# Optimization experiments

Hardware: AMD Instinct MI355X
Metric: run time of the kernel (lower is better)

## Reference

```python
import jax, jax.numpy as jnp
import numpy as np

EPS = 1e-6
LN_EPS = 1e-6


def _bd(x, W):
    # Block-diagonal dense: x (B, F) viewed as (B, H, D); W (H, D, D)
    B = x.shape[0]
    H, D, _ = W.shape
    return jnp.einsum('bhd,hde->bhe', x.reshape(B, H, D), W).reshape(B, H * D)


def setup_inputs() -> dict:
    key = jax.random.key(0)
    B, F, H, D, K = 4096, 1024, 4, 256, 4
    ks = jax.random.split(key, 24)
    inp = {}
    inp['inputs'] = jax.random.normal(ks[0], (B, F), jnp.float32)
    inp['c'] = jax.random.normal(ks[1], (B, F), jnp.float32)
    inp['n'] = jax.random.uniform(ks[2], (B, F), jnp.float32)  # nonzero -> general stabilizer branch
    inp['m'] = jax.random.normal(ks[3], (B, F), jnp.float32)
    inp['h'] = jax.random.normal(ks[4], (B, F), jnp.float32)
    inp['conv_state'] = jax.random.normal(ks[5], (B, K, F), jnp.float32)
    inp['conv_kernel'] = jax.random.normal(ks[6], (K, F), jnp.float32) * 0.1
    inp['conv_bias'] = jax.random.normal(ks[7], (F,), jnp.float32) * 0.1
    for idx, name in enumerate(['Wi', 'Wf', 'Wz', 'Wo', 'Ri', 'Rf', 'Rz', 'Ro']):
        inp[name] = jax.random.normal(ks[8 + idx], (H, D, D), jnp.float32) * 0.02
    for idx, name in enumerate(['bi', 'bf', 'bz', 'bo']):
        inp[name] = jax.random.normal(ks[16 + idx], (F,), jnp.float32) * 0.1
    inp['ln_scale'] = jnp.ones((H, D), jnp.float32)
    return inp


def reference(inputs, c, n, m, h, conv_state, conv_kernel, conv_bias,
              Wi, Wf, Wz, Wo, Ri, Rf, Rz, Ro, bi, bf, bz, bo, ln_scale):
    B = inputs.shape[0]
    H, D = ln_scale.shape

    # Causal depthwise conv, single step: shift state, append new input
    new_conv_state = jnp.concatenate([conv_state[:, 1:, :], inputs[:, None, :]], axis=1)  # (B,K,F)
    conv_x = jnp.einsum('bkf,kf->bf', new_conv_state, conv_kernel) + conv_bias
    conv_act = jax.nn.silu(conv_x)

    # Gate pre-activations: input (block-diag) + recurrent (block-diag) + bias
    i = _bd(conv_act, Wi) + _bd(h, Ri) + bi
    f = _bd(conv_act, Wf) + _bd(h, Rf) + bf
    z = _bd(inputs, Wz) + _bd(h, Rz) + bz
    o = _bd(inputs, Wo) + _bd(h, Ro) + bo

    o_gate = jax.nn.sigmoid(o)
    log_f = -jax.nn.softplus(-f)  # forget_activation == 'sigmoid'

    # Stabilizer
    m_new = jnp.where(jnp.all(n == 0.0), i, jnp.maximum(log_f + m, i))
    i_p = jnp.minimum(jnp.exp(i - m_new), 1.0)
    f_p = jnp.minimum(jnp.exp(log_f + m - m_new), 1.0)

    c_new = f_p * c + i_p * jnp.tanh(z)
    n_new = f_p * n + i_p
    h_new = o_gate * (c_new / jnp.maximum(n_new, EPS))

    # Multi-head LayerNorm over head_dim (scale only, no bias)
    y = h_new.reshape(B, H, D)
    mu = jnp.mean(y, axis=-1, keepdims=True)
    var = jnp.var(y, axis=-1, keepdims=True)
    out = ((y - mu) * jax.lax.rsqrt(var + LN_EPS) * ln_scale).reshape(B, H * D)

    return (out, c_new, n_new, m_new, h_new, new_conv_state)
```

## Files before the change

kernel.cpp:

```cpp
#include <hip/hip_runtime.h>

#define B_N 4096
#define F_N 1024
#define H_N 4
#define D_N 256
#define BF_ELEMS (B_N * F_N)

typedef unsigned short u16;
typedef __bf16 bf16x8 __attribute__((ext_vector_type(8)));
typedef float f32x4 __attribute__((ext_vector_type(4)));
typedef u16 u16x4 __attribute__((ext_vector_type(4)));

__device__ __forceinline__ u16 f2bf(float v) {
    union { float f; unsigned u; } x; x.f = v;
    unsigned r = x.u + 0x7fffu + ((x.u >> 16) & 1u);
    return (u16)(r >> 16);
}

__global__ void kzero_flag(int* flag) {
    if (threadIdx.x == 0) *flag = 0;
}

__global__ void kflag(const float* __restrict__ n, int* __restrict__ flag) {
    int idx = blockIdx.x * 256 + threadIdx.x;
    const f32x4 v = *(const f32x4*)(n + idx * 4);
    bool any = (v[0] != 0.f) || (v[1] != 0.f) || (v[2] != 0.f) || (v[3] != 0.f);
    unsigned long long msk = __ballot(any);
    if (msk && (threadIdx.x & 63) == 0) *flag = 1;
}

__global__ void kconv(const float* __restrict__ inputs, const float* __restrict__ cs,
                      const float* __restrict__ ck, const float* __restrict__ cb,
                      const float* __restrict__ h,
                      float* __restrict__ ncs_out, u16* __restrict__ convact,
                      u16* __restrict__ hbf, u16* __restrict__ inbf) {
    int idx = blockIdx.x * 256 + threadIdx.x;
    int flat = idx << 2;
    int b = flat >> 10;
    int f = flat & 1023;
    const f32x4 x  = *(const f32x4*)(inputs + flat);
    const f32x4 c1 = *(const f32x4*)(cs + b * 4096 + 1024 + f);
    const f32x4 c2 = *(const f32x4*)(cs + b * 4096 + 2048 + f);
    const f32x4 c3 = *(const f32x4*)(cs + b * 4096 + 3072 + f);
    const f32x4 k0 = *(const f32x4*)(ck + f);
    const f32x4 k1 = *(const f32x4*)(ck + 1024 + f);
    const f32x4 k2 = *(const f32x4*)(ck + 2048 + f);
    const f32x4 k3 = *(const f32x4*)(ck + 3072 + f);
    const f32x4 bias = *(const f32x4*)(cb + f);
    const f32x4 h4 = *(const f32x4*)(h + flat);

    u16x4 ca, hb, ib;
    #pragma unroll
    for (int q = 0; q < 4; ++q) {
        float v = c1[q] * k0[q] + c2[q] * k1[q] + c3[q] * k2[q] + x[q] * k3[q] + bias[q];
        float a = v / (1.f + expf(-v));
        ca[q] = f2bf(a);
        hb[q] = f2bf(h4[q]);
        ib[q] = f2bf(x[q]);
    }
    *(u16x4*)(convact + flat) = ca;
    *(u16x4*)(hbf + flat) = hb;
    *(u16x4*)(inbf + flat) = ib;

    float* ob = ncs_out + b * 4096 + f;
    *(f32x4*)(ob)        = c1;
    *(f32x4*)(ob + 1024) = c2;
    *(f32x4*)(ob + 2048) = c3;
    *(f32x4*)(ob + 3072) = x;
}

__global__ void kconvw(const float* W0, const float* W1, const float* W2, const float* W3,
                       const float* W4, const float* W5, const float* W6, const float* W7,
                       u16* __restrict__ wt) {
    const float* tab[8] = {W0, W1, W2, W3, W4, W5, W6, W7};
    int mat = blockIdx.z;
    int hd = blockIdx.y;
    const float* src = tab[mat] + hd * 65536;
    u16* dst = wt + (mat * 4 + hd) * 65536;
    __shared__ float tile[32][33];
    int tx = threadIdx.x & 31, ty = threadIdx.x >> 5;
    int bx = (blockIdx.x & 7) * 32;
    int by = (blockIdx.x >> 3) * 32;
    #pragma unroll
    for (int r = 0; r < 4; ++r)
        tile[ty + r * 8][tx] = src[(by + ty + r * 8) * 256 + bx + tx];
    __syncthreads();
    #pragma unroll
    for (int r = 0; r < 4; ++r)
        dst[(bx + ty + r * 8) * 256 + by + tx] = f2bf(tile[tx][ty + r * 8]);
}

__global__ __launch_bounds__(256) void kgemm(
    const u16* __restrict__ convact, const u16* __restrict__ inbf,
    const u16* __restrict__ hbf, const u16* __restrict__ wt,
    float* __restrict__ gates) {
    __shared__ u16 ldsA[128 * 32];
    __shared__ u16 ldsB[64 * 32];

    int t = threadIdx.x;
    int mtile = blockIdx.x;
    int nt = blockIdx.y;
    int z = blockIdx.z;
    int pass = z >> 2;
    int hd = z & 3;
    int gsel = pass * 2 + (nt >> 2);
    int e0 = (nt & 3) * 64;
    int row0 = mtile * 128;

    const u16* a0 = (pass ? inbf : convact) + row0 * 1024 + hd * 256;
    const u16* a1 = hbf + row0 * 1024 + hd * 256;
    const u16* b0 = wt + (gsel * 4 + hd) * 65536 + e0 * 256;
    const u16* b1 = wt + ((gsel + 4) * 4 + hd) * 65536 + e0 * 256;

    f32x4 acc[4][2];
    #pragma unroll
    for (int i = 0; i < 4; ++i)
        #pragma unroll
        for (int j = 0; j < 2; ++j)
            acc[i][j] = (f32x4){0.f, 0.f, 0.f, 0.f};

    int lane = t & 63;
    int lr = lane & 15, lk = lane >> 4;
    int w = t >> 6;
    int wm = w >> 1, wn = w & 1;
    int wbase = t & ~63;

    for (int ks = 0; ks < 16; ++ks) {
        int kk = ks * 32;
        const u16* ap = (kk < 256) ? (a0 + kk) : (a1 + (kk - 256));
        const u16* bp = (kk < 256) ? (b0 + kk) : (b1 + (kk - 256));
        __syncthreads();
        #pragma unroll
        for (int s = 0; s < 2; ++s) {
            int idx = t + s * 256;
            int row = idx >> 2, seg = idx & 3;
            __builtin_amdgcn_global_load_lds(
                (const __attribute__((address_space(1))) void*)(ap + row * 1024 + seg * 8),
                (__attribute__((address_space(3))) void*)(&ldsA[(wbase + s * 256) * 8]),
                16, 0, 0);
        }
        {
            int row = t >> 2, seg = t & 3;
            __builtin_amdgcn_global_load_lds(
                (const __attribute__((address_space(1))) void*)(bp + row * 256 + seg * 8),
                (__attribute__((address_space(3))) void*)(&ldsB[wbase * 8]),
                16, 0, 0);
        }
        __syncthreads();

        bf16x8 a[4], bfr[2];
        #pragma unroll
        for (int mi = 0; mi < 4; ++mi)
            a[mi] = *(const bf16x8*)&ldsA[(wm * 64 + mi * 16 + lr) * 32 + lk * 8];
        #pragma unroll
        for (int ni = 0; ni < 2; ++ni)
            bfr[ni] = *(const bf16x8*)&ldsB[(wn * 32 + ni * 16 + lr) * 32 + lk * 8];
        #pragma unroll
        for (int mi = 0; mi < 4; ++mi)
            #pragma unroll
            for (int ni = 0; ni < 2; ++ni)
                acc[mi][ni] = __builtin_amdgcn_mfma_f32_16x16x32_bf16(a[mi], bfr[ni], acc[mi][ni], 0, 0, 0);
    }

    float* gout = gates + (size_t)gsel * BF_ELEMS;
    #pragma unroll
    for (int mi = 0; mi < 4; ++mi)
        #pragma unroll
        for (int ni = 0; ni < 2; ++ni)
            #pragma unroll
            for (int r = 0; r < 4; ++r) {
                int row = row0 + wm * 64 + mi * 16 + lk * 4 + r;
                int col = hd * 256 + e0 + wn * 32 + ni * 16 + lr;
                gout[row * 1024 + col] = acc[mi][ni][r];
            }
}

__global__ __launch_bounds__(256) void kpoint(
    const float* __restrict__ gates,
    const float* __restrict__ c, const float* __restrict__ n, const float* __restrict__ m,
    const float* __restrict__ bgi, const float* __restrict__ bgf,
    const float* __restrict__ bgz, const float* __restrict__ bgo,
    const float* __restrict__ ln_scale, const int* __restrict__ flagp,
    float* __restrict__ out) {
    int b = blockIdx.x;
    int t = threadIdx.x;
    int l = t & 63;
    int j = (t >> 6) * 256 + l * 4;
    int idx = b * 1024 + j;
    int flag = *flagp;

    f32x4 iv = *(const f32x4*)(gates + idx);
    f32x4 fv = *(const f32x4*)(gates + (size_t)BF_ELEMS + idx);
    f32x4 zv = *(const f32x4*)(gates + 2 * (size_t)BF_ELEMS + idx);
    f32x4 ov = *(const f32x4*)(gates + 3 * (size_t)BF_ELEMS + idx);
    f32x4 b_i = *(const f32x4*)(bgi + j);
    f32x4 b_f = *(const f32x4*)(bgf + j);
    f32x4 b_z = *(const f32x4*)(bgz + j);
    f32x4 b_o = *(const f32x4*)(bgo + j);
    f32x4 cv = *(const f32x4*)(c + idx);
    f32x4 nv = *(const f32x4*)(n + idx);
    f32x4 mv = *(const f32x4*)(m + idx);
    f32x4 sc = *(const f32x4*)(ln_scale + j);

    f32x4 cn, nn, mn, hn;
    float s = 0.f, ss = 0.f;
    #pragma unroll
    for (int q = 0; q < 4; ++q) {
        float I = iv[q] + b_i[q];
        float Fg = fv[q] + b_f[q];
        float Z = zv[q] + b_z[q];
        float O = ov[q] + b_o[q];
        float og = 1.f / (1.f + expf(-O));
        float lf = (Fg >= 0.f) ? -log1pf(expf(-Fg)) : (Fg - log1pf(expf(Fg)));
        float mnew = flag ? fmaxf(lf + mv[q], I) : I;
        float ip = fminf(expf(I - mnew), 1.f);
        float fp = fminf(expf(lf + mv[q] - mnew), 1.f);
        float cnew = fp * cv[q] + ip * tanhf(Z);
        float nnew = fp * nv[q] + ip;
        float hnew = og * (cnew / fmaxf(nnew, 1e-6f));
        cn[q] = cnew; nn[q] = nnew; mn[q] = mnew; hn[q] = hnew;
        s += hnew; ss += hnew * hnew;
    }
    #pragma unroll
    for (int off = 32; off >= 1; off >>= 1) {
        s  += __shfl_xor(s, off);
        ss += __shfl_xor(ss, off);
    }
    float mu = s * (1.f / 256.f);
    float var = ss * (1.f / 256.f) - mu * mu;
    float rs = rsqrtf(var + 1e-6f);

    f32x4 o4;
    #pragma unroll
    for (int q = 0; q < 4; ++q)
        o4[q] = (hn[q] - mu) * rs * sc[q];

    *(f32x4*)(out + idx) = o4;
    *(f32x4*)(out + (size_t)BF_ELEMS + idx) = cn;
    *(f32x4*)(out + 2 * (size_t)BF_ELEMS + idx) = nn;
    *(f32x4*)(out + 3 * (size_t)BF_ELEMS + idx) = mn;
    *(f32x4*)(out + 4 * (size_t)BF_ELEMS + idx) = hn;
}

extern "C" void kernel_launch(void* const* d_in, const int* in_sizes, int n_in,
                              void* d_out, int out_size, void* d_ws, size_t ws_size,
                              hipStream_t stream) {
    const float* inputs = (const float*)d_in[0];
    const float* c = (const float*)d_in[1];
    const float* n = (const float*)d_in[2];
    const float* m = (const float*)d_in[3];
    const float* h = (const float*)d_in[4];
    const float* conv_state = (const float*)d_in[5];
    const float* conv_kernel = (const float*)d_in[6];
    const float* conv_bias = (const float*)d_in[7];
    const float* W[8];
    for (int i = 0; i < 8; ++i) W[i] = (const float*)d_in[8 + i];
    const float* bgi = (const float*)d_in[16];
    const float* bgf = (const float*)d_in[17];
    const float* bgz = (const float*)d_in[18];
    const float* bgo = (const float*)d_in[19];
    const float* ln_scale = (const float*)d_in[20];
    float* out = (float*)d_out;

    char* ws = (char*)d_ws;
    int* flag = (int*)ws;
    u16* convact = (u16*)(ws + 256);
    u16* hbf = convact + BF_ELEMS;
    u16* inbf = hbf + BF_ELEMS;
    u16* wt = inbf + BF_ELEMS;
    float* gates = (float*)(ws + 256 + (size_t)3 * BF_ELEMS * 2 + (size_t)8 * 4 * 65536 * 2);

    kzero_flag<<<1, 64, 0, stream>>>(flag);
    kflag<<<4096, 256, 0, stream>>>(n, flag);
    kconv<<<4096, 256, 0, stream>>>(inputs, conv_state, conv_kernel, conv_bias, h,
                                    out + 5 * (size_t)BF_ELEMS, convact, hbf, inbf);
    kconvw<<<dim3(64, 4, 8), 256, 0, stream>>>(W[0], W[1], W[2], W[3], W[4], W[5], W[6], W[7], wt);
    kgemm<<<dim3(32, 8, 8), 256, 0, stream>>>(convact, inbf, hbf, wt, gates);
    kpoint<<<4096, 256, 0, stream>>>(gates, c, n, m, bgi, bgf, bgz, bgo, ln_scale, flag, out);
}
```

Before: 135.4 us.

## Widen GEMM N-tile, fuse bias into epilogue, store gate preactivations as bf16

New measurement: 127.0 us. 1.07x faster.

```diff
diff --git a/kernel.cpp b/kernel.cpp
--- a/kernel.cpp
+++ b/kernel.cpp
@@ -15,6 +15,11 @@
     union { float f; unsigned u; } x; x.f = v;
     unsigned r = x.u + 0x7fffu + ((x.u >> 16) & 1u);
     return (u16)(r >> 16);
+}
+
+__device__ __forceinline__ float bf2f(u16 v) {
+    union { unsigned u; float f; } x; x.u = ((unsigned)v) << 16;
+    return x.f;
 }
 
 __global__ void kzero_flag(int* flag) {
@@ -93,9 +98,11 @@
 __global__ __launch_bounds__(256) void kgemm(
     const u16* __restrict__ convact, const u16* __restrict__ inbf,
     const u16* __restrict__ hbf, const u16* __restrict__ wt,
-    float* __restrict__ gates) {
+    const float* __restrict__ bgi, const float* __restrict__ bgf,
+    const float* __restrict__ bgz, const float* __restrict__ bgo,
+    u16* __restrict__ gates16) {
     __shared__ u16 ldsA[128 * 32];
-    __shared__ u16 ldsB[64 * 32];
+    __shared__ u16 ldsB[128 * 32];
 
     int t = threadIdx.x;
     int mtile = blockIdx.x;
@@ -103,20 +110,22 @@
     int z = blockIdx.z;
     int pass = z >> 2;
     int hd = z & 3;
-    int gsel = pass * 2 + (nt >> 2);
-    int e0 = (nt & 3) * 64;
+    int gsel = pass * 2 + (nt >> 1);
+    int e0 = (nt & 1) * 128;
     int row0 = mtile * 128;
 
     const u16* a0 = (pass ? inbf : convact) + row0 * 1024 + hd * 256;
     const u16* a1 = hbf + row0 * 1024 + hd * 256;
     const u16* b0 = wt + (gsel * 4 + hd) * 65536 + e0 * 256;
     const u16* b1 = wt + ((gsel + 4) * 4 + hd) * 65536 + e0 * 256;
-
-    f32x4 acc[4][2];
+    const float* btab[4] = {bgi, bgf, bgz, bgo};
+    const float* bias = btab[gsel] + hd * 256 + e0;
+
+    f32x4 acc[4][4];
     #pragma unroll
     for (int i = 0; i < 4; ++i)
         #pragma unroll
-        for (int j = 0; j < 2; ++j)
+        for (int j = 0; j < 4; ++j)
             acc[i][j] = (f32x4){0.f, 0.f, 0.f, 0.f};
 
     int lane = t & 63;
@@ -139,47 +148,52 @@
                 (__attribute__((address_space(3))) void*)(&ldsA[(wbase + s * 256) * 8]),
                 16, 0, 0);
         }
-        {
-            int row = t >> 2, seg = t & 3;
+        #pragma unroll
+        for (int s = 0; s < 2; ++s) {
+            int idx = t + s * 256;
+            int row = idx >> 2, seg = idx & 3;
             __builtin_amdgcn_global_load_lds(
                 (const __attribute__((address_space(1))) void*)(bp + row * 256 + seg * 8),
-                (__attribute__((address_space(3))) void*)(&ldsB[wbase * 8]),
+                (__attribute__((address_space(3))) void*)(&ldsB[(wbase + s * 256) * 8]),
                 16, 0, 0);
         }
         __syncthreads();
 
-        bf16x8 a[4], bfr[2];
+        bf16x8 a[4], bfr[4];
         #pragma unroll
         for (int mi = 0; mi < 4; ++mi)
             a[mi] = *(const bf16x8*)&ldsA[(wm * 64 + mi * 16 + lr) * 32 + lk * 8];
         #pragma unroll
-        for (int ni = 0; ni < 2; ++ni)
-            bfr[ni] = *(const bf16x8*)&ldsB[(wn * 32 + ni * 16 + lr) * 32 + lk * 8];
+        for (int ni = 0; ni < 4; ++ni)
+            bfr[ni] = *(const bf16x8*)&ldsB[(wn * 64 + ni * 16 + lr) * 32 + lk * 8];
         #pragma unroll
         for (int mi = 0; mi < 4; ++mi)
             #pragma unroll
-            for (int ni = 0; ni < 2; ++ni)
+            for (int ni = 0; ni < 4; ++ni)
                 acc[mi][ni] = __builtin_amdgcn_mfma_f32_16x16x32_bf16(a[mi], bfr[ni], acc[mi][ni], 0, 0, 0);
     }
 
-    float* gout = gates + (size_t)gsel * BF_ELEMS;
+    float bv[4];
+    #pragma unroll
+    for (int ni = 0; ni < 4; ++ni)
+        bv[ni] = bias[wn * 64 + ni * 16 + lr];
+
+    u16* gout = gates16 + (size_t)gsel * BF_ELEMS;
     #pragma unroll
     for (int mi = 0; mi < 4; ++mi)
         #pragma unroll
-        for (int ni = 0; ni < 2; ++ni)
+        for (int ni = 0; ni < 4; ++ni)
             #pragma unroll
             for (int r = 0; r < 4; ++r) {
                 int row = row0 + wm * 64 + mi * 16 + lk * 4 + r;
-                int col = hd * 256 + e0 + wn * 32 + ni * 16 + lr;
-                gout[row * 1024 + col] = acc[mi][ni][r];
+                int col = hd * 256 + e0 + wn * 64 + ni * 16 + lr;
+                gout[row * 1024 + col] = f2bf(acc[mi][ni][r] + bv[ni]);
             }
 }
 
 __global__ __launch_bounds__(256) void kpoint(
-    const float* __restrict__ gates,
+    const u16* __restrict__ gates16,
     const float* __restrict__ c, const float* __restrict__ n, const float* __restrict__ m,
-    const float* __restrict__ bgi, const float* __restrict__ bgf,
-    const float* __restrict__ bgz, const float* __restrict__ bgo,
     const float* __restrict__ ln_scale, const int* __restrict__ flagp,
     float* __restrict__ out) {
     int b = blockIdx.x;
@@ -189,14 +203,10 @@
     int idx = b * 1024 + j;
     int flag = *flagp;
 
-    f32x4 iv = *(const f32x4*)(gates + idx);
-    f32x4 fv = *(const f32x4*)(gates + (size_t)BF_ELEMS + idx);
-    f32x4 zv = *(const f32x4*)(gates + 2 * (size_t)BF_ELEMS + idx);
-    f32x4 ov = *(const f32x4*)(gates + 3 * (size_t)BF_ELEMS + idx);
-    f32x4 b_i = *(const f32x4*)(bgi + j);
-    f32x4 b_f = *(const f32x4*)(bgf + j);
-    f32x4 b_z = *(const f32x4*)(bgz + j);
-    f32x4 b_o = *(const f32x4*)(bgo + j);
+    u16x4 iv = *(const u16x4*)(gates16 + idx);
+    u16x4 fv = *(const u16x4*)(gates16 + (size_t)BF_ELEMS + idx);
+    u16x4 zv = *(const u16x4*)(gates16 + 2 * (size_t)BF_ELEMS + idx);
+    u16x4 ov = *(const u16x4*)(gates16 + 3 * (size_t)BF_ELEMS + idx);
     f32x4 cv = *(const f32x4*)(c + idx);
     f32x4 nv = *(const f32x4*)(n + idx);
     f32x4 mv = *(const f32x4*)(m + idx);
@@ -206,10 +216,10 @@
     float s = 0.f, ss = 0.f;
     #pragma unroll
     for (int q = 0; q < 4; ++q) {
-        float I = iv[q] + b_i[q];
-        float Fg = fv[q] + b_f[q];
-        float Z = zv[q] + b_z[q];
-        float O = ov[q] + b_o[q];
+        float I = bf2f(iv[q]);
+        float Fg = bf2f(fv[q]);
+        float Z = bf2f(zv[q]);
+        float O = bf2f(ov[q]);
         float og = 1.f / (1.f + expf(-O));
         float lf = (Fg >= 0.f) ? -log1pf(expf(-Fg)) : (Fg - log1pf(expf(Fg)));
         float mnew = flag ? fmaxf(lf + mv[q], I) : I;
@@ -268,13 +278,14 @@
     u16* hbf = convact + BF_ELEMS;
     u16* inbf = hbf + BF_ELEMS;
     u16* wt = inbf + BF_ELEMS;
-    float* gates = (float*)(ws + 256 + (size_t)3 * BF_ELEMS * 2 + (size_t)8 * 4 * 65536 * 2);
+    u16* gates16 = wt + (size_t)8 * 4 * 65536;
 
     kzero_flag<<<1, 64, 0, stream>>>(flag);
     kflag<<<4096, 256, 0, stream>>>(n, flag);
     kconv<<<4096, 256, 0, stream>>>(inputs, conv_state, conv_kernel, conv_bias, h,
                                     out + 5 * (size_t)BF_ELEMS, convact, hbf, inbf);
     kconvw<<<dim3(64, 4, 8), 256, 0, stream>>>(W[0], W[1], W[2], W[3], W[4], W[5], W[6], W[7], wt);
-    kgemm<<<dim3(32, 8, 8), 256, 0, stream>>>(convact, inbf, hbf, wt, gates);
-    kpoint<<<4096, 256, 0, stream>>>(gates, c, n, m, bgi, bgf, bgz, bgo, ln_scale, flag, out);
-}
+    kgemm<<<dim3(32, 4, 8), 256, 0, stream>>>(convact, inbf, hbf, wt,
+                                              bgi, bgf, bgz, bgo, gates16);
+    kpoint<<<4096, 256, 0, stream>>>(gates16, c, n, m, ln_scale, flag, out);
+}
```
